# Optimization experiments

Measured on AMD Instinct MI355X. Metric: run time of the kernel, lower is better.

The kernel has to match this reference:

```python
import jax, jax.numpy as jnp
import numpy as np

B, S, DM = 2, 1024, 2048
H, HD, RD = 16, 128, 64
DQL, DKVL = 384, 512
THETA = 10000.0
EPS = 1e-6


def _rope_tables(seq, dim, theta):
    freqs = 1.0 / (theta ** (jnp.arange(0, dim, 2, dtype=jnp.float32) / dim))  # (dim//2,)
    t = jnp.arange(seq, dtype=jnp.float32)
    ang = jnp.outer(t, freqs)  # (seq, dim//2)
    return jnp.cos(ang), jnp.sin(ang)


def _apply_rope(x, cos, sin):
    # x: (B, S, H, D), consecutive pairs treated as complex (llama-style)
    xr = x.reshape(x.shape[:-1] + (-1, 2))
    xe, xo = xr[..., 0], xr[..., 1]
    c = cos[None, :, None, :]
    s = sin[None, :, None, :]
    return jnp.stack([xe * c - xo * s, xe * s + xo * c], axis=-1).reshape(x.shape)


def _rmsnorm(x, w):
    return x * jax.lax.rsqrt(jnp.mean(x * x, axis=-1, keepdims=True) + EPS) * w


def setup_inputs() -> dict:
    key = jax.random.key(0)
    ks = jax.random.split(key, 9)
    sc = 0.02
    return {
        "x": jax.random.normal(ks[0], (B, S, DM), dtype=jnp.float32),
        "Wq_down": jax.random.normal(ks[1], (DM, DQL), dtype=jnp.float32) * sc,
        "q_norm_w": jnp.ones((DQL,), dtype=jnp.float32),
        "Wq_up": jax.random.normal(ks[2], (DQL, H * HD), dtype=jnp.float32) * sc,
        "Wq_rope": jax.random.normal(ks[3], (DM, H * RD), dtype=jnp.float32) * sc,
        "Wkv_down": jax.random.normal(ks[4], (DM, DKVL), dtype=jnp.float32) * sc,
        "kv_norm_w": jnp.ones((DKVL,), dtype=jnp.float32),
        "Wk_up": jax.random.normal(ks[5], (DKVL, H * HD), dtype=jnp.float32) * sc,
        "Wv_up": jax.random.normal(ks[6], (DKVL, H * HD), dtype=jnp.float32) * sc,
        "Wk_rope": jax.random.normal(ks[7], (DM, H * RD), dtype=jnp.float32) * sc,
        "Wout": jax.random.normal(ks[8], (H * HD, DM), dtype=jnp.float32) * sc,
    }


def reference(x, Wq_down, q_norm_w, Wq_up, Wq_rope, Wkv_down, kv_norm_w,
              Wk_up, Wv_up, Wk_rope, Wout):
    b, s, _ = x.shape
    cos, sin = _rope_tables(s, RD, THETA)

    # --- query path: low-rank compression + RMSNorm + up-projection ---
    c_q = _rmsnorm(x @ Wq_down, q_norm_w)                       # (b, s, d_q_latent)
    q = (c_q @ Wq_up).reshape(b, s, H, HD).transpose(0, 2, 1, 3)  # (b, h, s, hd)
    q_rope = _apply_rope((x @ Wq_rope).reshape(b, s, H, RD), cos, sin)
    q_rope = q_rope.transpose(0, 2, 1, 3)                        # (b, h, s, rd)

    # --- kv path: latent compression + RMSNorm, reconstruct K/V ---
    c_kv = _rmsnorm(x @ Wkv_down, kv_norm_w)                     # (b, s, d_kv_latent)
    k = (c_kv @ Wk_up).reshape(b, s, H, HD).transpose(0, 2, 1, 3)
    v = (c_kv @ Wv_up).reshape(b, s, H, HD).transpose(0, 2, 1, 3)
    k_rope = _apply_rope((x @ Wk_rope).reshape(b, s, H, RD), cos, sin)
    k_rope = k_rope.transpose(0, 2, 1, 3)

    # --- attention: content scores + decoupled rope scores ---
    scale = (HD + RD) ** -0.5
    scores = (jnp.einsum('bhqd,bhkd->bhqk', q, k)
              + jnp.einsum('bhqd,bhkd->bhqk', q_rope, k_rope)) * scale
    attn = jax.nn.softmax(scores, axis=-1)                       # (b, h, s, s)

    out = jnp.einsum('bhqk,bhkd->bhqd', attn, v)                 # (b, h, s, hd)
    out = out.transpose(0, 2, 1, 3).reshape(b, s, H * HD) @ Wout # (b, s, d_model)
    return out, attn
```

## Files before the change

kernel.cpp:

```cpp
#include <hip/hip_runtime.h>

#define B_    2
#define S_    1024
#define DM_   2048
#define H_    16
#define HD_   128
#define RD_   64
#define DQL_  384
#define DKVL_ 512
#define NTOK  (B_*S_)
#define CATD  (HD_+RD_)
#define LDSZ  (128*64)

typedef float f32x4 __attribute__((ext_vector_type(4)));
typedef short s16x8 __attribute__((ext_vector_type(8)));
typedef unsigned int u32;

__device__ __forceinline__ unsigned short f2b(float f) {
  u32 u = __float_as_uint(f);
  u = (u + 0x7FFFu + ((u >> 16) & 1u)) >> 16;
  return (unsigned short)u;
}
__device__ __forceinline__ f32x4 mfma16(s16x8 a, s16x8 b, f32x4 c) {
  return __builtin_amdgcn_mfma_f32_16x16x32_bf16(a, b, c, 0, 0, 0);
}
__device__ __forceinline__ void gl_lds16(const void* g, void* l) {
  __builtin_amdgcn_global_load_lds((const __attribute__((address_space(1))) u32*)g,
                                   (__attribute__((address_space(3))) u32*)l, 16, 0, 0);
}

__device__ __forceinline__ void gemm_core(const unsigned short* __restrict__ Ag,
                                          const unsigned short* __restrict__ Bg,
                                          int K,
                                          unsigned short (&As)[2][LDSZ],
                                          unsigned short (&Bs)[2][LDSZ],
                                          f32x4 (&acc)[4][2]) {
  const int tid = threadIdx.x;
  const int wave = tid >> 6, lane = tid & 63;
  const int wr = (wave >> 2) * 64, wc = (wave & 3) * 32;
  const int l16 = lane & 15, kg = lane >> 4;
  int sr[2], sc[2];
#pragma unroll
  for (int i = 0; i < 2; ++i) {
    const int g = i * 512 + tid;
    sr[i] = g >> 3;
    sc[i] = ((g & 7) ^ (sr[i] & 7)) * 8;
  }
  auto STAGE = [&](int b, int k0) {
#pragma unroll
    for (int i = 0; i < 2; ++i) {
      gl_lds16(Ag + (size_t)sr[i] * K + k0 + sc[i], (void*)&As[b][(i * 512 + tid) * 8]);
      gl_lds16(Bg + (size_t)sr[i] * K + k0 + sc[i], (void*)&Bs[b][(i * 512 + tid) * 8]);
    }
  };
  STAGE(0, 0);
  int cur = 0;
  for (int k0 = 0; k0 < K; k0 += 64) {
    __syncthreads();
    if (k0 + 64 < K) STAGE(cur ^ 1, k0 + 64);
#pragma unroll
    for (int kk = 0; kk < 2; ++kk) {
      const int sl = ((kk * 4 + kg) ^ (l16 & 7)) * 8;
      s16x8 af[4], bf2[2];
#pragma unroll
      for (int i = 0; i < 4; ++i)
        af[i] = *reinterpret_cast<const s16x8*>(&As[cur][(wr + i * 16 + l16) * 64 + sl]);
#pragma unroll
      for (int i = 0; i < 2; ++i)
        bf2[i] = *reinterpret_cast<const s16x8*>(&Bs[cur][(wc + i * 16 + l16) * 64 + sl]);
#pragma unroll
      for (int mi = 0; mi < 4; ++mi)
#pragma unroll
        for (int ni = 0; ni < 2; ++ni)
          acc[mi][ni] = mfma16(af[mi], bf2[ni], acc[mi][ni]);
    }
    cur ^= 1;
  }
}

__global__ __launch_bounds__(256) void k_rope_tab(float2* __restrict__ csT) {
  const int i = blockIdx.x * 256 + threadIdx.x;
  const int s = i >> 5, p = i & 31;
  const float freq = powf(10000.0f, -(float)p / 32.0f);
  float sn, cs;
  sincosf((float)s * freq, &sn, &cs);
  csT[i] = make_float2(cs, sn);
}

__global__ __launch_bounds__(256) void k_f2b(const float* __restrict__ in,
                                             unsigned short* __restrict__ out, int n4) {
  int i = blockIdx.x * 256 + threadIdx.x;
  if (i >= n4) return;
  const float4 v = reinterpret_cast<const float4*>(in)[i];
  ushort4 o;
  o.x = f2b(v.x); o.y = f2b(v.y); o.z = f2b(v.z); o.w = f2b(v.w);
  reinterpret_cast<ushort4*>(out)[i] = o;
}

struct TD { const float* in; unsigned short* out; int R, C, blk0; float scale; };
struct TD8 { TD d[8]; };
__global__ __launch_bounds__(256) void k_transpose_all(TD8 descs) {
  __shared__ float tile[64][65];
  const int bid = blockIdx.x;
  int di = 0;
#pragma unroll
  for (int i = 1; i < 8; ++i) if (bid >= descs.d[i].blk0) di = i;
  const TD dd = descs.d[di];
  const int local = bid - dd.blk0;
  const int tiles_r = dd.R >> 6;
  const int tr_ = local % tiles_r, tc_ = local / tiles_r;
  const int r0 = tr_ * 64, c0 = tc_ * 64;
  const int t = threadIdx.x;
  const int tr = t >> 4, tc4 = (t & 15) * 4;
#pragma unroll
  for (int i = 0; i < 4; ++i) {
    const int rr = tr + i * 16;
    const float4 v = *reinterpret_cast<const float4*>(dd.in + (size_t)(r0 + rr) * dd.C + c0 + tc4);
    tile[rr][tc4 + 0] = v.x; tile[rr][tc4 + 1] = v.y;
    tile[rr][tc4 + 2] = v.z; tile[rr][tc4 + 3] = v.w;
  }
  __syncthreads();
#pragma unroll
  for (int i = 0; i < 4; ++i) {
    const int oc = tr + i * 16;
    ushort4 o;
    o.x = f2b(tile[tc4 + 0][oc] * dd.scale); o.y = f2b(tile[tc4 + 1][oc] * dd.scale);
    o.z = f2b(tile[tc4 + 2][oc] * dd.scale); o.w = f2b(tile[tc4 + 3][oc] * dd.scale);
    *reinterpret_cast<ushort4*>(dd.out + (size_t)(c0 + oc) * dd.R + r0 + tc4) = o;
  }
}

__global__ __launch_bounds__(512, 2) void k_gemm2(const unsigned short* __restrict__ A,
                                                  const unsigned short* __restrict__ Bt,
                                                  float* __restrict__ C,
                                                  int M, int N, int K) {
  __shared__ unsigned short As[2][LDSZ];
  __shared__ unsigned short Bs[2][LDSZ];
  const int nwg = gridDim.x * gridDim.y;
  int id = blockIdx.y * gridDim.x + blockIdx.x;
  id = (id & 7) * (nwg >> 3) + (id >> 3);
  const int tm = (id % gridDim.x) * 128;
  const int tn = (id / gridDim.x) * 128;
  const int tid = threadIdx.x;
  const int wave = tid >> 6, lane = tid & 63;
  const int wr = (wave >> 2) * 64, wc = (wave & 3) * 32;
  const int l16 = lane & 15, kg = lane >> 4;

  f32x4 acc[4][2] = {};
  gemm_core(A + (size_t)tm * K, Bt + (size_t)tn * K, K, As, Bs, acc);

#pragma unroll
  for (int mi = 0; mi < 4; ++mi)
#pragma unroll
    for (int ni = 0; ni < 2; ++ni) {
      const int rr = tm + wr + mi * 16 + kg * 4;
      const int cc = tn + wc + ni * 16 + l16;
#pragma unroll
      for (int j = 0; j < 4; ++j)
        C[(size_t)(rr + j) * N + cc] = acc[mi][ni][j];
    }
}

__global__ __launch_bounds__(512, 2) void k_proj_a(const unsigned short* __restrict__ xb,
                                                   const unsigned short* __restrict__ WdT,
                                                   const unsigned short* __restrict__ WrT,
                                                   float* __restrict__ cdown,
                                                   unsigned short* __restrict__ Qcat,
                                                   unsigned short* __restrict__ Kcat,
                                                   const float2* __restrict__ csT) {
  __shared__ unsigned short As[2][LDSZ];
  __shared__ unsigned short Bs[2][LDSZ];
  int id = blockIdx.x;
  id = (id & 7) * 46 + (id >> 3);
  const bool down = id < 112;
  int gm, tn; const unsigned short* Bt;
  if (down) { gm = id % 16; tn = (id / 16) * 128; Bt = WdT; }
  else { const int i2 = id - 112; gm = i2 % 16; tn = (i2 / 16) * 128; Bt = WrT; }
  const int tm = gm * 128;

  const int tid = threadIdx.x;
  const int wave = tid >> 6, lane = tid & 63;
  const int wr = (wave >> 2) * 64, wc = (wave & 3) * 32;
  const int l16 = lane & 15, kg = lane >> 4;

  f32x4 acc[4][2] = {};
  gemm_core(xb + (size_t)tm * DM_, Bt + (size_t)tn * DM_, DM_, As, Bs, acc);

  if (down) {
#pragma unroll
    for (int mi = 0; mi < 4; ++mi)
#pragma unroll
      for (int ni = 0; ni < 2; ++ni) {
        const int rr = tm + wr + mi * 16 + kg * 4;
        const int cc = tn + wc + ni * 16 + l16;
#pragma unroll
        for (int j = 0; j < 4; ++j)
          cdown[(size_t)(rr + j) * (DQL_ + DKVL_) + cc] = acc[mi][ni][j];
      }
  } else {
#pragma unroll
    for (int mi = 0; mi < 4; ++mi)
#pragma unroll
      for (int ni = 0; ni < 2; ++ni) {
        const int col = tn + wc + ni * 16 + l16;
        unsigned short* dst = (col < 1024) ? Qcat : Kcat;
        const int c1 = col & 1023;
        const int hh = c1 >> 6, dd2 = c1 & 63, p = dd2 >> 1, odd = dd2 & 1;
        const int row0 = tm + wr + mi * 16 + kg * 4;
#pragma unroll
        for (int j = 0; j < 4; ++j) {
          const float own = acc[mi][ni][j];
          const float prt = __shfl_xor(own, 1, 64);
          const int tok = row0 + j, b = tok >> 10, s = tok & 1023;
          const float2 cs = csT[s * 32 + p];
          const float o = odd ? (prt * cs.y + own * cs.x) : (own * cs.x - prt * cs.y);
          dst[((size_t)(b * H_ + hh) * S_ + s) * CATD + HD_ + dd2] = f2b(o);
        }
      }
  }
}

__global__ __launch_bounds__(512, 2) void k_proj_b(const unsigned short* __restrict__ cqb,
                                                   const unsigned short* __restrict__ ckvb,
                                                   const unsigned short* __restrict__ WqupT,
                                                   const unsigned short* __restrict__ WkvupT,
                                                   unsigned short* __restrict__ Qcat,
                                                   unsigned short* __restrict__ Kcat,
                                                   unsigned short* __restrict__ VTb) {
  __shared__ unsigned short As[2][LDSZ];
  __shared__ unsigned short Bs[2][LDSZ];
  int id = blockIdx.x;
  id = (id & 7) * 96 + (id >> 3);
  const bool qgrp = id < 256;
  int gm, tn, K; const unsigned short* Bt; const unsigned short* A;
  if (qgrp) { gm = id & 15; tn = (id >> 4) * 128; Bt = WqupT; A = cqb; K = DQL_; }
  else { const int i2 = id - 256; gm = i2 & 15; tn = (i2 >> 4) * 128; Bt = WkvupT; A = ckvb; K = DKVL_; }
  const int tm = gm * 128;

  const int tid = threadIdx.x;
  const int wave = tid >> 6, lane = tid & 63;
  const int wr = (wave >> 2) * 64, wc = (wave & 3) * 32;
  const int l16 = lane & 15, kg = lane >> 4;

  f32x4 acc[4][2] = {};
  gemm_core(A + (size_t)tm * K, Bt + (size_t)tn * K, K, As, Bs, acc);

#pragma unroll
  for (int mi = 0; mi < 4; ++mi)
#pragma unroll
    for (int ni = 0; ni < 2; ++ni) {
      const int col = tn + wc + ni * 16 + l16;
      const int row0 = tm + wr + mi * 16 + kg * 4;
      if (qgrp || col < 2048) {
        unsigned short* dst = qgrp ? Qcat : Kcat;
        const int hh = (col & 2047) >> 7, d = col & 127;
#pragma unroll
        for (int j = 0; j < 4; ++j) {
          const int tok = row0 + j, b = tok >> 10, s = tok & 1023;
          dst[((size_t)(b * H_ + hh) * S_ + s) * CATD + d] = f2b(acc[mi][ni][j]);
        }
      } else {
        const int m2 = col - 2048;
        const int hh = m2 >> 7, d = m2 & 127;
        const int b = row0 >> 10, s0 = row0 & 1023;
        ushort4 o;
        o.x = f2b(acc[mi][ni][0]); o.y = f2b(acc[mi][ni][1]);
        o.z = f2b(acc[mi][ni][2]); o.w = f2b(acc[mi][ni][3]);
        *reinterpret_cast<ushort4*>(&VTb[((size_t)(b * H_ + hh) * HD_ + d) * S_ + s0]) = o;
      }
    }
}

__global__ __launch_bounds__(64) void k_rmsnorm(const float* __restrict__ in, int stride,
                                                const float* __restrict__ w,
                                                unsigned short* __restrict__ out, int D) {
  const int row = blockIdx.x;
  const float* x = in + (size_t)row * stride;
  float ss = 0.f;
  for (int i = threadIdx.x; i < D; i += 64) { const float v = x[i]; ss = fmaf(v, v, ss); }
#pragma unroll
  for (int off = 32; off; off >>= 1) ss += __shfl_xor(ss, off, 64);
  const float r = rsqrtf(ss / (float)D + 1e-6f);
  for (int i = threadIdx.x; i < D; i += 64)
    out[(size_t)row * D + i] = f2b(x[i] * r * w[i]);
}

#define KVB 64
__global__ __launch_bounds__(512, 4) void k_attn3(const unsigned short* __restrict__ Qcat,
                                                  const unsigned short* __restrict__ Kcat,
                                                  const unsigned short* __restrict__ VT,
                                                  float* __restrict__ attn_out,
                                                  unsigned short* __restrict__ ctx) {
  __shared__ unsigned short Ks[2][KVB * 192];
  __shared__ unsigned short Vs[128 * 64];
  __shared__ unsigned short Pl[8][16 * 64];
  const int d0 = blockIdx.x;
  const int xcd = d0 & 7, i0 = d0 >> 3;
  const int bh = xcd | ((i0 >> 3) << 3);
  const int qc = i0 & 7;
  const int b = bh >> 4, h = bh & 15;

  const int tid = threadIdx.x, wave = tid >> 6, lane = tid & 63;
  const int l16 = lane & 15, kg = lane >> 4;
  const int qw = qc * 128 + wave * 16;

  const unsigned short* Qb = Qcat + ((size_t)bh * S_ + qw) * CATD;
  s16x8 qf[6];
#pragma unroll
  for (int ks = 0; ks < 6; ++ks)
    qf[ks] = *reinterpret_cast<const s16x8*>(Qb + (size_t)l16 * CATD + ks * 32 + kg * 8);

  int srk[3], sck[3];
#pragma unroll
  for (int j = 0; j < 3; ++j) {
    const int s = j * 512 + tid;
    srk[j] = s / 24;
    sck[j] = ((s % 24) ^ (srk[j] & 7)) * 8;
  }
  const unsigned short* Kb = Kcat + (size_t)bh * S_ * CATD;
  auto STAGE_K = [&](int bb, int ch) {
    const unsigned short* Kc = Kb + (size_t)ch * KVB * CATD;
#pragma unroll
    for (int j = 0; j < 3; ++j)
      gl_lds16(Kc + (size_t)srk[j] * CATD + sck[j], (void*)&Ks[bb][(j * 512 + tid) * 8]);
  };

  const unsigned short* Vb = VT + (size_t)bh * HD_ * S_;
  int srv[2], scv[2];
#pragma unroll
  for (int i = 0; i < 2; ++i) {
    const int g = i * 512 + tid;
    srv[i] = g >> 3;
    scv[i] = ((g & 7) ^ (srv[i] & 7)) * 8;
  }
  auto STAGE_V = [&](int ch) {
#pragma unroll
    for (int i = 0; i < 2; ++i)
      gl_lds16(Vb + (size_t)srv[i] * S_ + ch * KVB + scv[i], (void*)&Vs[(i * 512 + tid) * 8]);
  };

  f32x4 oacc[8] = {};
  float mx = -1e30f, sm = 0.f, rl = 0.f;

  STAGE_K(0, 0);
  int cur = 0;
  for (int g = 0; g < 32; ++g) {
    __syncthreads();
    const int ch = g & 15;
    const bool p2 = g >= 16;
    if (p2) STAGE_V(ch);
    if (g < 31) STAGE_K(cur ^ 1, (g + 1) & 15);

    f32x4 acc[4] = {};
#pragma unroll
    for (int ni = 0; ni < 4; ++ni) {
      const int row = ni * 16 + l16;
#pragma unroll
      for (int ks = 0; ks < 6; ++ks) {
        const int slot = (ks * 4 + kg) ^ (l16 & 7);
        const s16x8 af = *reinterpret_cast<const s16x8*>(&Ks[cur][row * 192 + slot * 8]);
        acc[ni] = mfma16(af, qf[ks], acc[ni]);
      }
    }

    if (!p2) {
      float cm = -1e30f;
#pragma unroll
      for (int ni = 0; ni < 4; ++ni)
#pragma unroll
        for (int j = 0; j < 4; ++j) cm = fmaxf(cm, acc[ni][j]);
      const float nm = fmaxf(mx, cm);
      sm *= __expf(mx - nm);
#pragma unroll
      for (int ni = 0; ni < 4; ++ni)
#pragma unroll
        for (int j = 0; j < 4; ++j) sm += __expf(acc[ni][j] - nm);
      mx = nm;
      if (g == 15) {
#pragma unroll
        for (int off = 16; off < 64; off <<= 1) {
          const float om = __shfl_xor(mx, off, 64);
          const float os = __shfl_xor(sm, off, 64);
          const float nm2 = fmaxf(mx, om);
          sm = sm * __expf(mx - nm2) + os * __expf(om - nm2);
          mx = nm2;
        }
        rl = 1.0f / sm;
      }
    } else {
      if (g < 31) asm volatile("s_waitcnt vmcnt(3)" ::: "memory");
      else        asm volatile("s_waitcnt vmcnt(0)" ::: "memory");
      __builtin_amdgcn_s_barrier();
      __builtin_amdgcn_sched_barrier(0);

      float* Ao = attn_out + ((size_t)bh * S_ + qw + l16) * S_ + ch * KVB;
      unsigned short* Pw = &Pl[wave][0];
#pragma unroll
      for (int ni = 0; ni < 4; ++ni) {
        float4 w4;
        w4.x = __expf(acc[ni][0] - mx) * rl;
        w4.y = __expf(acc[ni][1] - mx) * rl;
        w4.z = __expf(acc[ni][2] - mx) * rl;
        w4.w = __expf(acc[ni][3] - mx) * rl;
        *reinterpret_cast<float4*>(Ao + ni * 16 + kg * 4) = w4;
        ushort4 pb;
        pb.x = f2b(w4.x); pb.y = f2b(w4.y); pb.z = f2b(w4.z); pb.w = f2b(w4.w);
        *reinterpret_cast<ushort4*>(&Pw[l16 * 64 + (((ni * 4 + kg) ^ l16) * 4)]) = pb;
      }
#pragma unroll
      for (int kk = 0; kk < 2; ++kk) {
        const short4 lo = *reinterpret_cast<const short4*>(&Pw[l16 * 64 + (((kk * 8 + kg * 2 + 0) ^ l16) * 4)]);
        const short4 hi = *reinterpret_cast<const short4*>(&Pw[l16 * 64 + (((kk * 8 + kg * 2 + 1) ^ l16) * 4)]);
        s16x8 pa;
        pa[0] = lo.x; pa[1] = lo.y; pa[2] = lo.z; pa[3] = lo.w;
        pa[4] = hi.x; pa[5] = hi.y; pa[6] = hi.z; pa[7] = hi.w;
#pragma unroll
        for (int ni = 0; ni < 8; ++ni) {
          const int row = ni * 16 + l16;
          const s16x8 vf = *reinterpret_cast<const s16x8*>(
              &Vs[row * 64 + (((kk * 4 + kg) ^ (l16 & 7)) * 8)]);
          oacc[ni] = mfma16(pa, vf, oacc[ni]);
        }
      }
    }
    cur ^= 1;
  }

#pragma unroll
  for (int ni = 0; ni < 8; ++ni)
#pragma unroll
    for (int j = 0; j < 4; ++j)
      ctx[((size_t)(b * S_ + qw + kg * 4 + j)) * DM_ + h * HD_ + ni * 16 + l16] =
          f2b(oacc[ni][j]);
}

extern "C" void kernel_launch(void* const* d_in, const int* in_sizes, int n_in,
                              void* d_out, int out_size, void* d_ws, size_t ws_size,
                              hipStream_t stream) {
  const float* x         = (const float*)d_in[0];
  const float* Wq_down   = (const float*)d_in[1];
  const float* q_norm_w  = (const float*)d_in[2];
  const float* Wq_up     = (const float*)d_in[3];
  const float* Wq_rope   = (const float*)d_in[4];
  const float* Wkv_down  = (const float*)d_in[5];
  const float* kv_norm_w = (const float*)d_in[6];
  const float* Wk_up     = (const float*)d_in[7];
  const float* Wv_up     = (const float*)d_in[8];
  const float* Wk_rope   = (const float*)d_in[9];
  const float* Wout      = (const float*)d_in[10];

  float* out0 = (float*)d_out;
  float* attn = out0 + (size_t)B_ * S_ * DM_;

  char* ws = (char*)d_ws;
  size_t off = 0;
  auto alloc = [&](size_t bytes) -> void* {
    void* p = ws + off;
    off += (bytes + 255) & ~(size_t)255;
    return p;
  };

  unsigned short* xb     = (unsigned short*)alloc((size_t)NTOK * DM_ * 2);
  unsigned short* WdT    = (unsigned short*)alloc((size_t)(DQL_ + DKVL_) * DM_ * 2);
  unsigned short* WrT    = (unsigned short*)alloc((size_t)DM_ * DM_ * 2);
  unsigned short* WqupT  = (unsigned short*)alloc((size_t)DM_ * DQL_ * 2);
  unsigned short* WkvupT = (unsigned short*)alloc((size_t)(2 * DM_) * DKVL_ * 2);
  unsigned short* WoutT  = (unsigned short*)alloc((size_t)DM_ * DM_ * 2);
  float* cdown           = (float*)alloc((size_t)NTOK * (DQL_ + DKVL_) * 4);
  unsigned short* cqb    = (unsigned short*)alloc((size_t)NTOK * DQL_ * 2);
  unsigned short* ckvb   = (unsigned short*)alloc((size_t)NTOK * DKVL_ * 2);
  unsigned short* Qcat   = (unsigned short*)alloc((size_t)B_ * H_ * S_ * CATD * 2);
  unsigned short* Kcat   = (unsigned short*)alloc((size_t)B_ * H_ * S_ * CATD * 2);
  unsigned short* VTb    = (unsigned short*)alloc((size_t)B_ * H_ * HD_ * S_ * 2);
  unsigned short* ctxb   = (unsigned short*)alloc((size_t)NTOK * DM_ * 2);
  float2* csT            = (float2*)alloc((size_t)S_ * 32 * sizeof(float2));

  if (off > ws_size) return;

  const float qsc = 0.07216878364870323f;

  k_rope_tab<<<128, 256, 0, stream>>>(csT);
  k_f2b<<<(NTOK * DM_ / 4 + 255) / 256, 256, 0, stream>>>(x, xb, NTOK * DM_ / 4);

  TD8 td;
  int blk0 = 0;
  auto setd = [&](int i, const float* in, unsigned short* out, int R, int C, float sc) {
    td.d[i] = TD{in, out, R, C, blk0, sc};
    blk0 += (R >> 6) * (C >> 6);
  };
  setd(0, Wq_down,  WdT,                        DM_,  DQL_,  1.0f);
  setd(1, Wkv_down, WdT + (size_t)DQL_ * DM_,   DM_,  DKVL_, 1.0f);
  setd(2, Wq_rope,  WrT,                        DM_,  1024,  qsc);
  setd(3, Wk_rope,  WrT + (size_t)1024 * DM_,   DM_,  1024,  1.0f);
  setd(4, Wq_up,    WqupT,                      DQL_, DM_,   qsc);
  setd(5, Wk_up,    WkvupT,                     DKVL_, DM_,  1.0f);
  setd(6, Wv_up,    WkvupT + (size_t)DM_ * DKVL_, DKVL_, DM_, 1.0f);
  setd(7, Wout,     WoutT,                      DM_,  DM_,   1.0f);
  k_transpose_all<<<blk0, 256, 0, stream>>>(td);

  k_proj_a<<<368, 512, 0, stream>>>(xb, WdT, WrT, cdown, Qcat, Kcat, csT);
  k_rmsnorm<<<NTOK, 64, 0, stream>>>(cdown,        DQL_ + DKVL_, q_norm_w,  cqb,  DQL_);
  k_rmsnorm<<<NTOK, 64, 0, stream>>>(cdown + DQL_, DQL_ + DKVL_, kv_norm_w, ckvb, DKVL_);

  k_proj_b<<<768, 512, 0, stream>>>(cqb, ckvb, WqupT, WkvupT, Qcat, Kcat, VTb);

  k_attn3<<<256, 512, 0, stream>>>(Qcat, Kcat, VTb, attn, ctxb);

  k_gemm2<<<dim3(NTOK / 128, DM_ / 128), 512, 0, stream>>>(ctxb, WoutT, out0, NTOK, DM_, DM_);
}
```

Measured before the change: 211.2 us.

## Shrink GEMM and attention workgroups to 256 threads and fuse prep kernels

Changes the GEMM core tile from 128x128 to 128x64 with 4 waves per workgroup, doubling grid sizes for proj_a, proj_b and the output GEMM. Attention now uses 256-thread blocks covering 64 queries each. The rope-table, cast and transpose kernels are merged into one launch, and the two rmsnorm launches become one. The aim is better CU occupancy and load balance plus fewer launches, at the cost of less B-tile reuse per workgroup and more redundant A loads.

```diff
diff --git a/kernel.cpp b/kernel.cpp
--- a/kernel.cpp
+++ b/kernel.cpp
@@ -10,7 +10,8 @@
 #define DKVL_ 512
 #define NTOK  (B_*S_)
 #define CATD  (HD_+RD_)
-#define LDSZ  (128*64)
+#define LDSA  (128*64)
+#define LDSB  (64*64)
 
 typedef float f32x4 __attribute__((ext_vector_type(4)));
 typedef short s16x8 __attribute__((ext_vector_type(8)));
@@ -32,26 +33,33 @@
 __device__ __forceinline__ void gemm_core(const unsigned short* __restrict__ Ag,
                                           const unsigned short* __restrict__ Bg,
                                           int K,
-                                          unsigned short (&As)[2][LDSZ],
-                                          unsigned short (&Bs)[2][LDSZ],
+                                          unsigned short (&As)[2][LDSA],
+                                          unsigned short (&Bs)[2][LDSB],
                                           f32x4 (&acc)[4][2]) {
   const int tid = threadIdx.x;
   const int wave = tid >> 6, lane = tid & 63;
-  const int wr = (wave >> 2) * 64, wc = (wave & 3) * 32;
+  const int wr = (wave >> 1) * 64, wc = (wave & 1) * 32;
   const int l16 = lane & 15, kg = lane >> 4;
-  int sr[2], sc[2];
+  int sra[4], sca[4], srb[2], scb[2];
+#pragma unroll
+  for (int i = 0; i < 4; ++i) {
+    const int g = i * 256 + tid;
+    sra[i] = g >> 3;
+    sca[i] = ((g & 7) ^ (sra[i] & 7)) * 8;
+  }
 #pragma unroll
   for (int i = 0; i < 2; ++i) {
-    const int g = i * 512 + tid;
-    sr[i] = g >> 3;
-    sc[i] = ((g & 7) ^ (sr[i] & 7)) * 8;
+    const int g = i * 256 + tid;
+    srb[i] = g >> 3;
+    scb[i] = ((g & 7) ^ (srb[i] & 7)) * 8;
   }
   auto STAGE = [&](int b, int k0) {
 #pragma unroll
-    for (int i = 0; i < 2; ++i) {
-      gl_lds16(Ag + (size_t)sr[i] * K + k0 + sc[i], (void*)&As[b][(i * 512 + tid) * 8]);
-      gl_lds16(Bg + (size_t)sr[i] * K + k0 + sc[i], (void*)&Bs[b][(i * 512 + tid) * 8]);
-    }
+    for (int i = 0; i < 4; ++i)
+      gl_lds16(Ag + (size_t)sra[i] * K + k0 + sca[i], (void*)&As[b][(i * 256 + tid) * 8]);
+#pragma unroll
+    for (int i = 0; i < 2; ++i)
+      gl_lds16(Bg + (size_t)srb[i] * K + k0 + scb[i], (void*)&Bs[b][(i * 256 + tid) * 8]);
   };
   STAGE(0, 0);
   int cur = 0;
@@ -78,30 +86,31 @@
   }
 }
 
-__global__ __launch_bounds__(256) void k_rope_tab(float2* __restrict__ csT) {
-  const int i = blockIdx.x * 256 + threadIdx.x;
-  const int s = i >> 5, p = i & 31;
-  const float freq = powf(10000.0f, -(float)p / 32.0f);
-  float sn, cs;
-  sincosf((float)s * freq, &sn, &cs);
-  csT[i] = make_float2(cs, sn);
-}
-
-__global__ __launch_bounds__(256) void k_f2b(const float* __restrict__ in,
-                                             unsigned short* __restrict__ out, int n4) {
-  int i = blockIdx.x * 256 + threadIdx.x;
-  if (i >= n4) return;
-  const float4 v = reinterpret_cast<const float4*>(in)[i];
-  ushort4 o;
-  o.x = f2b(v.x); o.y = f2b(v.y); o.z = f2b(v.z); o.w = f2b(v.w);
-  reinterpret_cast<ushort4*>(out)[i] = o;
-}
-
 struct TD { const float* in; unsigned short* out; int R, C, blk0; float scale; };
 struct TD8 { TD d[8]; };
-__global__ __launch_bounds__(256) void k_transpose_all(TD8 descs) {
+__global__ __launch_bounds__(256) void k_prep(TD8 descs, float2* __restrict__ csT,
+                                              const float* __restrict__ x,
+                                              unsigned short* __restrict__ xb) {
   __shared__ float tile[64][65];
   const int bid = blockIdx.x;
+  const int t = threadIdx.x;
+  if (bid < 128) {
+    const int i = bid * 256 + t;
+    const int s = i >> 5, p = i & 31;
+    const float freq = powf(10000.0f, -(float)p / 32.0f);
+    float sn, cs;
+    sincosf((float)s * freq, &sn, &cs);
+    csT[i] = make_float2(cs, sn);
+    return;
+  }
+  if (bid >= 3328) {
+    const int i = (bid - 3328) * 256 + t;
+    const float4 v = reinterpret_cast<const float4*>(x)[i];
+    ushort4 o;
+    o.x = f2b(v.x); o.y = f2b(v.y); o.z = f2b(v.z); o.w = f2b(v.w);
+    reinterpret_cast<ushort4*>(xb)[i] = o;
+    return;
+  }
   int di = 0;
 #pragma unroll
   for (int i = 1; i < 8; ++i) if (bid >= descs.d[i].blk0) di = i;
@@ -110,7 +119,6 @@
   const int tiles_r = dd.R >> 6;
   const int tr_ = local % tiles_r, tc_ = local / tiles_r;
   const int r0 = tr_ * 64, c0 = tc_ * 64;
-  const int t = threadIdx.x;
   const int tr = t >> 4, tc4 = (t & 15) * 4;
 #pragma unroll
   for (int i = 0; i < 4; ++i) {
@@ -130,20 +138,21 @@
   }
 }
 
-__global__ __launch_bounds__(512, 2) void k_gemm2(const unsigned short* __restrict__ A,
+__global__ __launch_bounds__(256, 4) void k_gemm2(const unsigned short* __restrict__ A,
                                                   const unsigned short* __restrict__ Bt,
                                                   float* __restrict__ C,
                                                   int M, int N, int K) {
-  __shared__ unsigned short As[2][LDSZ];
-  __shared__ unsigned short Bs[2][LDSZ];
-  const int nwg = gridDim.x * gridDim.y;
-  int id = blockIdx.y * gridDim.x + blockIdx.x;
+  __shared__ unsigned short As[2][LDSA];
+  __shared__ unsigned short Bs[2][LDSB];
+  const int mt = M >> 7;
+  const int nwg = mt * (N >> 6);
+  int id = blockIdx.x;
   id = (id & 7) * (nwg >> 3) + (id >> 3);
-  const int tm = (id % gridDim.x) * 128;
-  const int tn = (id / gridDim.x) * 128;
+  const int tm = (id % mt) * 128;
+  const int tn = (id / mt) * 64;
   const int tid = threadIdx.x;
   const int wave = tid >> 6, lane = tid & 63;
-  const int wr = (wave >> 2) * 64, wc = (wave & 3) * 32;
+  const int wr = (wave >> 1) * 64, wc = (wave & 1) * 32;
   const int l16 = lane & 15, kg = lane >> 4;
 
   f32x4 acc[4][2] = {};
@@ -161,26 +170,26 @@
     }
 }
 
-__global__ __launch_bounds__(512, 2) void k_proj_a(const unsigned short* __restrict__ xb,
+__global__ __launch_bounds__(256, 4) void k_proj_a(const unsigned short* __restrict__ xb,
                                                    const unsigned short* __restrict__ WdT,
                                                    const unsigned short* __restrict__ WrT,
                                                    float* __restrict__ cdown,
                                                    unsigned short* __restrict__ Qcat,
                                                    unsigned short* __restrict__ Kcat,
                                                    const float2* __restrict__ csT) {
-  __shared__ unsigned short As[2][LDSZ];
-  __shared__ unsigned short Bs[2][LDSZ];
+  __shared__ unsigned short As[2][LDSA];
+  __shared__ unsigned short Bs[2][LDSB];
   int id = blockIdx.x;
-  id = (id & 7) * 46 + (id >> 3);
-  const bool down = id < 112;
+  id = (id & 7) * 92 + (id >> 3);
+  const bool down = id < 224;
   int gm, tn; const unsigned short* Bt;
-  if (down) { gm = id % 16; tn = (id / 16) * 128; Bt = WdT; }
-  else { const int i2 = id - 112; gm = i2 % 16; tn = (i2 / 16) * 128; Bt = WrT; }
+  if (down) { gm = id % 16; tn = (id / 16) * 64; Bt = WdT; }
+  else { const int i2 = id - 224; gm = i2 % 16; tn = (i2 / 16) * 64; Bt = WrT; }
   const int tm = gm * 128;
 
   const int tid = threadIdx.x;
   const int wave = tid >> 6, lane = tid & 63;
-  const int wr = (wave >> 2) * 64, wc = (wave & 3) * 32;
+  const int wr = (wave >> 1) * 64, wc = (wave & 1) * 32;
   const int l16 = lane & 15, kg = lane >> 4;
 
   f32x4 acc[4][2] = {};
@@ -220,26 +229,26 @@
   }
 }
 
-__global__ __launch_bounds__(512, 2) void k_proj_b(const unsigned short* __restrict__ cqb,
+__global__ __launch_bounds__(256, 4) void k_proj_b(const unsigned short* __restrict__ cqb,
                                                    const unsigned short* __restrict__ ckvb,
                                                    const unsigned short* __restrict__ WqupT,
                                                    const unsigned short* __restrict__ WkvupT,
                                                    unsigned short* __restrict__ Qcat,
                                                    unsigned short* __restrict__ Kcat,
                                                    unsigned short* __restrict__ VTb) {
-  __shared__ unsigned short As[2][LDSZ];
-  __shared__ unsigned short Bs[2][LDSZ];
+  __shared__ unsigned short As[2][LDSA];
+  __shared__ unsigned short Bs[2][LDSB];
   int id = blockIdx.x;
-  id = (id & 7) * 96 + (id >> 3);
-  const bool qgrp = id < 256;
+  id = (id & 7) * 192 + (id >> 3);
+  const bool qgrp = id < 512;
   int gm, tn, K; const unsigned short* Bt; const unsigned short* A;
-  if (qgrp) { gm = id & 15; tn = (id >> 4) * 128; Bt = WqupT; A = cqb; K = DQL_; }
-  else { const int i2 = id - 256; gm = i2 & 15; tn = (i2 >> 4) * 128; Bt = WkvupT; A = ckvb; K = DKVL_; }
+  if (qgrp) { gm = id & 15; tn = (id >> 4) * 64; Bt = WqupT; A = cqb; K = DQL_; }
+  else { const int i2 = id - 512; gm = i2 & 15; tn = (i2 >> 4) * 64; Bt = WkvupT; A = ckvb; K = DKVL_; }
   const int tm = gm * 128;
 
   const int tid = threadIdx.x;
   const int wave = tid >> 6, lane = tid & 63;
-  const int wr = (wave >> 2) * 64, wc = (wave & 3) * 32;
+  const int wr = (wave >> 1) * 64, wc = (wave & 1) * 32;
   const int l16 = lane & 15, kg = lane >> 4;
 
   f32x4 acc[4][2] = {};
@@ -271,38 +280,44 @@
     }
 }
 
-__global__ __launch_bounds__(64) void k_rmsnorm(const float* __restrict__ in, int stride,
-                                                const float* __restrict__ w,
-                                                unsigned short* __restrict__ out, int D) {
+__global__ __launch_bounds__(64) void k_rmsnorm2(const float* __restrict__ cdown,
+                                                 const float* __restrict__ qw,
+                                                 const float* __restrict__ kvw,
+                                                 unsigned short* __restrict__ cqb,
+                                                 unsigned short* __restrict__ ckvb) {
   const int row = blockIdx.x;
-  const float* x = in + (size_t)row * stride;
+  const bool isq = row < NTOK;
+  const int r = isq ? row : row - NTOK;
+  const int D = isq ? DQL_ : DKVL_;
+  const float* x = cdown + (size_t)r * (DQL_ + DKVL_) + (isq ? 0 : DQL_);
+  const float* w = isq ? qw : kvw;
+  unsigned short* out = (isq ? cqb : ckvb) + (size_t)r * D;
   float ss = 0.f;
   for (int i = threadIdx.x; i < D; i += 64) { const float v = x[i]; ss = fmaf(v, v, ss); }
 #pragma unroll
   for (int off = 32; off; off >>= 1) ss += __shfl_xor(ss, off, 64);
-  const float r = rsqrtf(ss / (float)D + 1e-6f);
-  for (int i = threadIdx.x; i < D; i += 64)
-    out[(size_t)row * D + i] = f2b(x[i] * r * w[i]);
+  const float rr = rsqrtf(ss / (float)D + 1e-6f);
+  for (int i = threadIdx.x; i < D; i += 64) out[i] = f2b(x[i] * rr * w[i]);
 }
 
 #define KVB 64
-__global__ __launch_bounds__(512, 4) void k_attn3(const unsigned short* __restrict__ Qcat,
+__global__ __launch_bounds__(256, 2) void k_attn3(const unsigned short* __restrict__ Qcat,
                                                   const unsigned short* __restrict__ Kcat,
                                                   const unsigned short* __restrict__ VT,
                                                   float* __restrict__ attn_out,
                                                   unsigned short* __restrict__ ctx) {
   __shared__ unsigned short Ks[2][KVB * 192];
   __shared__ unsigned short Vs[128 * 64];
-  __shared__ unsigned short Pl[8][16 * 64];
+  __shared__ unsigned short Pl[4][16 * 64];
   const int d0 = blockIdx.x;
   const int xcd = d0 & 7, i0 = d0 >> 3;
-  const int bh = xcd | ((i0 >> 3) << 3);
-  const int qc = i0 & 7;
+  const int bh = xcd + ((i0 >> 4) << 3);
+  const int qc = i0 & 15;
   const int b = bh >> 4, h = bh & 15;
 
   const int tid = threadIdx.x, wave = tid >> 6, lane = tid & 63;
   const int l16 = lane & 15, kg = lane >> 4;
-  const int qw = qc * 128 + wave * 16;
+  const int qw = qc * 64 + wave * 16;
 
   const unsigned short* Qb = Qcat + ((size_t)bh * S_ + qw) * CATD;
   s16x8 qf[6];
@@ -310,10 +325,10 @@
   for (int ks = 0; ks < 6; ++ks)
     qf[ks] = *reinterpret_cast<const s16x8*>(Qb + (size_t)l16 * CATD + ks * 32 + kg * 8);
 
-  int srk[3], sck[3];
-#pragma unroll
-  for (int j = 0; j < 3; ++j) {
-    const int s = j * 512 + tid;
+  int srk[6], sck[6];
+#pragma unroll
+  for (int j = 0; j < 6; ++j) {
+    const int s = j * 256 + tid;
     srk[j] = s / 24;
     sck[j] = ((s % 24) ^ (srk[j] & 7)) * 8;
   }
@@ -321,22 +336,22 @@
   auto STAGE_K = [&](int bb, int ch) {
     const unsigned short* Kc = Kb + (size_t)ch * KVB * CATD;
 #pragma unroll
-    for (int j = 0; j < 3; ++j)
-      gl_lds16(Kc + (size_t)srk[j] * CATD + sck[j], (void*)&Ks[bb][(j * 512 + tid) * 8]);
+    for (int j = 0; j < 6; ++j)
+      gl_lds16(Kc + (size_t)srk[j] * CATD + sck[j], (void*)&Ks[bb][(j * 256 + tid) * 8]);
   };
 
   const unsigned short* Vb = VT + (size_t)bh * HD_ * S_;
-  int srv[2], scv[2];
-#pragma unroll
-  for (int i = 0; i < 2; ++i) {
-    const int g = i * 512 + tid;
+  int srv[4], scv[4];
+#pragma unroll
+  for (int i = 0; i < 4; ++i) {
+    const int g = i * 256 + tid;
     srv[i] = g >> 3;
     scv[i] = ((g & 7) ^ (srv[i] & 7)) * 8;
   }
   auto STAGE_V = [&](int ch) {
 #pragma unroll
-    for (int i = 0; i < 2; ++i)
-      gl_lds16(Vb + (size_t)srv[i] * S_ + ch * KVB + scv[i], (void*)&Vs[(i * 512 + tid) * 8]);
+    for (int i = 0; i < 4; ++i)
+      gl_lds16(Vb + (size_t)srv[i] * S_ + ch * KVB + scv[i], (void*)&Vs[(i * 256 + tid) * 8]);
   };
 
   f32x4 oacc[8] = {};
@@ -388,7 +403,7 @@
         rl = 1.0f / sm;
       }
     } else {
-      if (g < 31) asm volatile("s_waitcnt vmcnt(3)" ::: "memory");
+      if (g < 31) asm volatile("s_waitcnt vmcnt(6)" ::: "memory");
       else        asm volatile("s_waitcnt vmcnt(0)" ::: "memory");
       __builtin_amdgcn_s_barrier();
       __builtin_amdgcn_sched_barrier(0);
@@ -479,11 +494,8 @@
 
   const float qsc = 0.07216878364870323f;
 
-  k_rope_tab<<<128, 256, 0, stream>>>(csT);
-  k_f2b<<<(NTOK * DM_ / 4 + 255) / 256, 256, 0, stream>>>(x, xb, NTOK * DM_ / 4);
-
   TD8 td;
-  int blk0 = 0;
+  int blk0 = 128;
   auto setd = [&](int i, const float* in, unsigned short* out, int R, int C, float sc) {
     td.d[i] = TD{in, out, R, C, blk0, sc};
     blk0 += (R >> 6) * (C >> 6);
@@ -496,15 +508,13 @@
   setd(5, Wk_up,    WkvupT,                     DKVL_, DM_,  1.0f);
   setd(6, Wv_up,    WkvupT + (size_t)DM_ * DKVL_, DKVL_, DM_, 1.0f);
   setd(7, Wout,     WoutT,                      DM_,  DM_,   1.0f);
-  k_transpose_all<<<blk0, 256, 0, stream>>>(td);
-
-  k_proj_a<<<368, 512, 0, stream>>>(xb, WdT, WrT, cdown, Qcat, Kcat, csT);
-  k_rmsnorm<<<NTOK, 64, 0, stream>>>(cdown,        DQL_ + DKVL_, q_norm_w,  cqb,  DQL_);
-  k_rmsnorm<<<NTOK, 64, 0, stream>>>(cdown + DQL_, DQL_ + DKVL_, kv_norm_w, ckvb, DKVL_);
-
-  k_proj_b<<<768, 512, 0, stream>>>(cqb, ckvb, WqupT, WkvupT, Qcat, Kcat, VTb);
-
-  k_attn3<<<256, 512, 0, stream>>>(Qcat, Kcat, VTb, attn, ctxb);
-
-  k_gemm2<<<dim3(NTOK / 128, DM_ / 128), 512, 0, stream>>>(ctxb, WoutT, out0, NTOK, DM_, DM_);
-}
+  k_prep<<<3328 + (NTOK * DM_ / 4) / 256, 256, 0, stream>>>(td, csT, x, xb);
+
+  k_proj_a<<<736, 256, 0, stream>>>(xb, WdT, WrT, cdown, Qcat, Kcat, csT);
+  k_rmsnorm2<<<2 * NTOK, 64, 0, stream>>>(cdown, q_norm_w, kv_norm_w, cqb, ckvb);
+  k_proj_b<<<1536, 256, 0, stream>>>(cqb, ckvb, WqupT, WkvupT, Qcat, Kcat, VTb);
+
+  k_attn3<<<512, 256, 0, stream>>>(Qcat, Kcat, VTb, attn, ctxb);
+
+  k_gemm2<<<512, 256, 0, stream>>>(ctxb, WoutT, out0, NTOK, DM_, DM_);
+}
```

Result: faster. 181.1 us (-14.2%).
